# Optimization experiments

Measured on AMD Instinct MI355X. Metric: run time of the kernel, lower is better.

Reference implementation:

```python
import jax, jax.numpy as jnp
import numpy as np

COMMITMENT = 1.0


def setup_inputs() -> dict:
    key = jax.random.key(0)
    k1, k2 = jax.random.split(key)
    input = jax.random.normal(k1, (8, 64, 64, 256), dtype=jnp.float32)
    embed = jax.random.normal(k2, (256, 8192), dtype=jnp.float32)  # [dim, n_embed]
    return {"input": input, "embed": embed}


def reference(input, embed):
    dim = embed.shape[0]
    flatten = input.reshape(-1, dim)  # [N, dim]
    dist = (
        jnp.sum(flatten * flatten, axis=1, keepdims=True)
        - 2.0 * (flatten @ embed)
        + jnp.sum(embed * embed, axis=0, keepdims=True)
    )
    embed_ind = jnp.argmin(dist, axis=1)  # == (-dist).max(1) indices
    embed_ind = embed_ind.reshape(input.shape[:-1])  # [B, H, W]
    quantize = jnp.take(embed.T, embed_ind, axis=0)  # codebook lookup [B,H,W,dim]
    loss = jnp.mean((jax.lax.stop_gradient(quantize) - input) ** 2) * COMMITMENT
    quantize = input + jax.lax.stop_gradient(quantize - input)  # straight-through
    return quantize, embed_ind, loss
```

## Files before the change

kernel.cpp:

```cpp
#include <hip/hip_runtime.h>
#include <hip/hip_fp16.h>

#define NROW 32768
#define DIM  256
#define NC   8192
#define CAP  16384
#define MARGINF 0.25f
#define BIAS 512.0f
#define AST 576
#define BST 576
#define LOSS_SCALE (1.0f / 8388608.0f)

typedef __attribute__((ext_vector_type(8))) _Float16 half8;
typedef __attribute__((ext_vector_type(4))) _Float16 half4;
typedef __attribute__((ext_vector_type(4))) float   floatx4;
typedef const __attribute__((address_space(1))) void* gas_p;
typedef __attribute__((address_space(3))) void*       las_p;

static __device__ __forceinline__ unsigned short f2hb(float f) {
    _Float16 h = (_Float16)f;
    unsigned short u;
    __builtin_memcpy(&u, &h, 2);
    return u;
}
static __device__ __forceinline__ unsigned umin_(unsigned a, unsigned b) { return a < b ? a : b; }
static __device__ __forceinline__ unsigned umax_(unsigned a, unsigned b) { return a > b ? a : b; }


__global__ void prep_a_k(const float* __restrict__ x, unsigned short* __restrict__ Ah,
                         float* __restrict__ norms) {
    int row  = blockIdx.x * 4 + (threadIdx.x >> 6);
    int lane = threadIdx.x & 63;
    const float4 v = ((const float4*)(x + (size_t)row * DIM))[lane];
    float s = v.x * v.x + v.y * v.y + v.z * v.z + v.w * v.w;
#pragma unroll
    for (int off = 32; off; off >>= 1) s += __shfl_down(s, off, 64);
    if (lane == 0) norms[row] = s;
    ushort4 hi4 = make_ushort4(f2hb(v.x), f2hb(v.y), f2hb(v.z), f2hb(v.w));
    ushort4 lo4 = make_ushort4(f2hb(v.x - (float)(_Float16)v.x),
                               f2hb(v.y - (float)(_Float16)v.y),
                               f2hb(v.z - (float)(_Float16)v.z),
                               f2hb(v.w - (float)(_Float16)v.w));
    unsigned short* rp = Ah + (size_t)row * AST;
    *(ushort4*)(rp + lane * 4)       = hi4;
    *(ushort4*)(rp + 288 + lane * 4) = lo4;
    if (lane < 8) {
        ushort4 ob = make_ushort4(0, 0, 0, 0);
        if (lane == 0) { ob.x = 0x3C00; ob.y = 0x3C00; }
        *(ushort4*)(rp + 256 + lane * 4) = ob;
    }
}

__global__ void code_norms_k(const float* __restrict__ e, unsigned short* __restrict__ Bh,
                             float* __restrict__ cHalf) {
    int j = blockIdx.x * 256 + threadIdx.x;
    float s = 0.f;
    for (int d = 0; d < DIM; ++d) { float v = e[(size_t)d * NC + j]; s += v * v; }
    cHalf[j] = 0.5f * s;
    float t = -0.5f * s - BIAS;
    unsigned short hi = f2hb(t);
    _Float16 hf; __builtin_memcpy(&hf, &hi, 2);
    unsigned short lo = f2hb(t - (float)hf);
    unsigned short* p = Bh + (size_t)j * BST + 256;
    p[0] = hi; p[1] = lo;
    for (int k2 = 2; k2 < 32; ++k2) p[k2] = 0;
}

__global__ void prep_b_k(const float* __restrict__ e, unsigned short* __restrict__ Bh) {
    __shared__ float t[32][33];
    int jb = blockIdx.x * 32, db = blockIdx.y * 32;
#pragma unroll
    for (int i = 0; i < 4; ++i)
        t[threadIdx.y + i * 8][threadIdx.x] =
            e[(size_t)(db + threadIdx.y + i * 8) * NC + jb + threadIdx.x];
    __syncthreads();
#pragma unroll
    for (int i = 0; i < 4; ++i) {
        int j = jb + threadIdx.y + i * 8;
        int d = db + threadIdx.x;
        float val = t[threadIdx.x][threadIdx.y + i * 8];
        Bh[(size_t)j * BST + d]       = f2hb(val);
        Bh[(size_t)j * BST + 288 + d] = f2hb(val - (float)(_Float16)val);
    }
}


#define WAITBAR asm volatile("s_waitcnt vmcnt(2) lgkmcnt(4)\n\ts_barrier" ::: "memory")

__global__ __launch_bounds__(512, 2) void vq_cheap_k(
    const unsigned short* __restrict__ Ah, const unsigned short* __restrict__ Bh,
    const float* __restrict__ cHalf,
    float* __restrict__ pv, int* __restrict__ pj, float* __restrict__ psv)
{
    __shared__ __align__(16) _Float16 Asl[8][4096];
    __shared__ __align__(16) _Float16 Bsl[4][8192];
    __shared__ float chl[2048];

    const int tid  = threadIdx.x;
    const int js   = blockIdx.x & 3;
    const int rb   = blockIdx.x >> 2;
    const int row0 = rb * 128, col0 = js * 2048;
    const int lane = tid & 63, l15 = lane & 15, lq = lane >> 4;
    const int wave = tid >> 6;
    const int wr = (wave >> 2) * 64;
    const int wc = (wave & 3) * 64;
    const int sr = tid >> 2;
    const int ks = (((tid & 3) ^ (sr & 3) ^ ((sr >> 2) & 3))) * 8;

    {
        float4 a = ((const float4*)(cHalf + col0))[tid];
        a.x += BIAS; a.y += BIAS; a.z += BIAS; a.w += BIAS;
        ((float4*)chl)[tid] = a;
    }

    const unsigned short* Abase = Ah + (size_t)(row0 + sr) * AST + ks;
#pragma unroll
    for (int c = 0; c < 8; ++c)
        __builtin_amdgcn_global_load_lds((gas_p)(Abase + c * 32), (las_p)&Asl[c][tid * 8], 16, 0, 0);

#define LOADB(JT_, C_, BUF_)                                                                  \
    do {                                                                                      \
        const unsigned short* bb_ = Bh + (size_t)(col0 + (JT_) * 256 + sr) * BST + (C_) * 32 + ks; \
        _Float16* lb_ = &Bsl[(BUF_)][tid * 8];                                                \
        __builtin_amdgcn_global_load_lds((gas_p)bb_,               (las_p)lb_,          16, 0, 0); \
        __builtin_amdgcn_global_load_lds((gas_p)(bb_ + 128 * BST), (las_p)(lb_ + 4096), 16, 0, 0); \
    } while (0)

    LOADB(0, 0, 0);
    LOADB(0, 1, 1);
    LOADB(0, 2, 2);

    unsigned k1[16], k2[16];
#pragma unroll
    for (int s = 0; s < 16; ++s) { k1[s] = 0xFFFFFFFFu; k2[s] = 0xFFFFFFFFu; }

    const floatx4 fzero = {0.0f, 0.0f, 0.0f, 0.0f};
    floatx4 acc[4][4];
#pragma unroll
    for (int rf = 0; rf < 4; ++rf)
#pragma unroll
        for (int cf = 0; cf < 4; ++cf) acc[rf][cf] = fzero;

    WAITBAR;

    half8 ar[4][4];
#pragma unroll
    for (int c = 0; c < 4; ++c)
#pragma unroll
        for (int rf = 0; rf < 4; ++rf) {
            const int m = wr + rf * 16 + l15;
            const int g = lq ^ (m & 3) ^ ((m >> 2) & 3);
            ar[c][rf] = *(const half8*)&Asl[c][m * 32 + g * 8];
        }

    half8 af[4], bf[4];
#pragma unroll
    for (int cf = 0; cf < 4; ++cf) {
        const int n = wc + cf * 16 + l15;
        const int g = lq ^ (n & 3) ^ ((n >> 2) & 3);
        bf[cf] = *(const half8*)&Bsl[0][n * 32 + g * 8];
    }

    for (int jt = 0; jt < 8; ++jt) {
#pragma unroll
        for (int c = 0; c < 8; ++c) {
            if (c <= 4) LOADB(jt, c + 3, (c + 3) & 3);
            else        LOADB((jt + 1) & 7, c - 5, (c + 3) & 3);

            __builtin_amdgcn_s_setprio(1);
            if (c < 4) {
#pragma unroll
                for (int rf = 0; rf < 4; ++rf)
#pragma unroll
                    for (int cf = 0; cf < 4; ++cf)
                        acc[rf][cf] = __builtin_amdgcn_mfma_f32_16x16x32_f16(
                            ar[c][rf], bf[cf], acc[rf][cf], 0, 0, 0);
            } else {
#pragma unroll
                for (int rf = 0; rf < 4; ++rf)
#pragma unroll
                    for (int cf = 0; cf < 4; ++cf)
                        acc[rf][cf] = __builtin_amdgcn_mfma_f32_16x16x32_f16(
                            af[rf], bf[cf], acc[rf][cf], 0, 0, 0);
            }
            __builtin_amdgcn_s_setprio(0);
            __builtin_amdgcn_sched_barrier(0);

            if (c == 7) {
#pragma unroll
                for (int cf = 0; cf < 4; ++cf) {
                    const unsigned colb = (unsigned)(jt * 256 + wc + cf * 16 + l15);
                    const float ch = chl[colb];
#pragma unroll
                    for (int rf = 0; rf < 4; ++rf)
#pragma unroll
                        for (int r = 0; r < 4; ++r) {
                            float s = acc[rf][cf][r] - ch;
                            unsigned key = (__float_as_uint(s) & 0xFFFFF800u) | colb;
                            int slot = rf * 4 + r;
                            unsigned t = umax_(key, k1[slot]);
                            k1[slot] = umin_(k1[slot], key);
                            k2[slot] = umin_(k2[slot], t);
                        }
                }
#pragma unroll
                for (int rf = 0; rf < 4; ++rf)
#pragma unroll
                    for (int cf = 0; cf < 4; ++cf) acc[rf][cf] = fzero;
            }

            if (((c + 1) & 7) >= 4) {
#pragma unroll
                for (int rf = 0; rf < 4; ++rf) {
                    const int m = wr + rf * 16 + l15;
                    const int g = lq ^ (m & 3) ^ ((m >> 2) & 3);
                    af[rf] = *(const half8*)&Asl[(c + 1) & 7][m * 32 + g * 8];
                }
            }
#pragma unroll
            for (int cf = 0; cf < 4; ++cf) {
                const int n = wc + cf * 16 + l15;
                const int g = lq ^ (n & 3) ^ ((n >> 2) & 3);
                bf[cf] = *(const half8*)&Bsl[(c + 1) & 3][n * 32 + g * 8];
            }

            WAITBAR;
        }
    }
#undef LOADB

#pragma unroll
    for (int st = 1; st < 16; st <<= 1) {
#pragma unroll
        for (int s = 0; s < 16; ++s) {
            unsigned o1 = (unsigned)__shfl_xor((int)k1[s], st, 64);
            unsigned o2 = (unsigned)__shfl_xor((int)k2[s], st, 64);
            unsigned t = umax_(k1[s], o1);
            k1[s] = umin_(k1[s], o1);
            k2[s] = umin_(umin_(k2[s], o2), t);
        }
    }

    __syncthreads();
    unsigned* mk1 = (unsigned*)&Asl[0][0];
    unsigned* mk2 = (unsigned*)&Asl[1][0];
    if (l15 == 0) {
#pragma unroll
        for (int rf = 0; rf < 4; ++rf)
#pragma unroll
            for (int r = 0; r < 4; ++r) {
                int rloc = wr + rf * 16 + lq * 4 + r;
                int slot = rf * 4 + r;
                mk1[rloc * 4 + (wave & 3)] = k1[slot];
                mk2[rloc * 4 + (wave & 3)] = k2[slot];
            }
    }
    __syncthreads();
    if (tid < 128) {
        unsigned a0 = mk1[tid * 4], a1 = mk1[tid * 4 + 1], a2 = mk1[tid * 4 + 2], a3 = mk1[tid * 4 + 3];
        unsigned x = umin_(a0, a1), y = umax_(a0, a1);
        unsigned z = umin_(a2, a3), w = umax_(a2, a3);
        unsigned m1  = umin_(x, z);
        unsigned sm1 = umin_(umax_(x, z), umin_(y, w));
        unsigned s0 = mk2[tid * 4], s1 = mk2[tid * 4 + 1], s2 = mk2[tid * 4 + 2], s3 = mk2[tid * 4 + 3];
        unsigned m2 = umin_(umin_(umin_(s0, s1), umin_(s2, s3)), sm1);
        pv[(size_t)js * NROW + row0 + tid]  = __uint_as_float(m1 & 0xFFFFF800u);
        pj[(size_t)js * NROW + row0 + tid]  = (int)(m1 & 2047u) + js * 2048;
        psv[(size_t)js * NROW + row0 + tid] = __uint_as_float(m2 & 0xFFFFF800u);
    }
}

#undef WAITBAR


template<bool RESCUE>
static __device__ __forceinline__ void chunk_off(int c, int& ac, int& bc) {
    if constexpr (RESCUE) {
        if (c < 8)       { ac = c * 32;              bc = c * 32; }
        else if (c < 16) { ac = (c - 8) * 32;        bc = 288 + (c - 8) * 32; }
        else             { ac = 288 + (c - 16) * 32; bc = (c - 16) * 32; }
    } else {
        ac = c * 32; bc = c * 32;
    }
}

template<int CHUNKS, int JT, int JSB, bool RESCUE>
__global__ __launch_bounds__(256, 2) void vq_gemm_k(
    const unsigned short* __restrict__ Ah, const unsigned short* __restrict__ Bh,
    const float* __restrict__ cHalf,
    float* __restrict__ pv, int* __restrict__ pj, float* __restrict__ psv,
    const int* __restrict__ list, const int* __restrict__ cnt)
{
    __shared__ __align__(16) _Float16 As[2][4096];
    __shared__ __align__(16) _Float16 Bs[2][4096];

    const int tid  = threadIdx.x;
    const int js   = blockIdx.x & ((1 << JSB) - 1);
    const int rb   = blockIdx.x >> JSB;
    const int row0 = rb * 128, col0 = js * (JT * 128);
    const int lane = tid & 63, l15 = lane & 15, lq = lane >> 4;
    const int wave = tid >> 6;
    const int wrow = (wave >> 1) * 64, wcol = (wave & 1) * 64;
    const int sr = tid >> 2, sp = (tid & 3) * 8;

    int nact = 0;
    if constexpr (RESCUE) {
        nact = *cnt;
        if (row0 >= nact) return;
    }

    const unsigned short *Abase0, *Abase1;
    if constexpr (RESCUE) {
        int i0 = row0 + sr, i1 = i0 + 64;
        int r0 = (i0 < nact) ? list[i0] : 0;
        int r1 = (i1 < nact) ? list[i1] : 0;
        Abase0 = Ah + (size_t)r0 * AST + sp;
        Abase1 = Ah + (size_t)r1 * AST + sp;
    } else {
        Abase0 = Ah + (size_t)(row0 + sr) * AST + sp;
        Abase1 = Abase0 + 64 * AST;
    }

    unsigned k1[16], k2[16];
    float bvf[16]; int bjf[16];
#pragma unroll
    for (int s = 0; s < 16; ++s) {
        k1[s] = 0xFFFFFFFFu; k2[s] = 0xFFFFFFFFu;
        bvf[s] = -3.4e38f; bjf[s] = 0;
    }

    const floatx4 fzero = {0.0f, 0.0f, 0.0f, 0.0f};
    floatx4 acc[4][4];
#pragma unroll
    for (int rf = 0; rf < 4; ++rf)
#pragma unroll
        for (int cf = 0; cf < 4; ++cf) acc[rf][cf] = fzero;

    const unsigned short* Bb = Bh + (size_t)(col0 + sr) * BST + sp;

#define LOAD4(AC, BC, BUF, BBASE)                                                            \
    do {                                                                                     \
        _Float16* la_ = &As[(BUF)][tid * 8];                                                 \
        _Float16* lb_ = &Bs[(BUF)][tid * 8];                                                 \
        __builtin_amdgcn_global_load_lds((gas_p)(Abase0 + (AC)),            (las_p)la_,          16, 0, 0); \
        __builtin_amdgcn_global_load_lds((gas_p)(Abase1 + (AC)),            (las_p)(la_ + 2048), 16, 0, 0); \
        __builtin_amdgcn_global_load_lds((gas_p)((BBASE) + (BC)),           (las_p)lb_,          16, 0, 0); \
        __builtin_amdgcn_global_load_lds((gas_p)((BBASE) + 64 * BST + (BC)),(las_p)(lb_ + 2048), 16, 0, 0); \
    } while (0)

    LOAD4(0, 0, 0, Bb);

    for (int jt = 0; jt < JT; ++jt) {
        const int p = (CHUNKS & 1) ? (jt & 1) : 0;
#pragma unroll
        for (int c = 0; c < CHUNKS; ++c) {
            const int buf = (c & 1) ^ p;
            __syncthreads();
            if (c + 1 < CHUNKS) {
                int an, bn;
                chunk_off<RESCUE>(c + 1, an, bn);
                LOAD4(an, bn, buf ^ 1, Bb);
            } else if (jt + 1 < JT) {
                LOAD4(0, 0, buf ^ 1, Bb + 128 * BST);
            }

            half8 af[4], bf[4];
#pragma unroll
            for (int rf = 0; rf < 4; ++rf)
                af[rf] = *(const half8*)&As[buf][(wrow + rf * 16 + l15) * 32 + lq * 8];
#pragma unroll
            for (int cf = 0; cf < 4; ++cf)
                bf[cf] = *(const half8*)&Bs[buf][(wcol + cf * 16 + l15) * 32 + lq * 8];
#pragma unroll
            for (int rf = 0; rf < 4; ++rf)
#pragma unroll
                for (int cf = 0; cf < 4; ++cf)
                    acc[rf][cf] = __builtin_amdgcn_mfma_f32_16x16x32_f16(
                        af[rf], bf[cf], acc[rf][cf], 0, 0, 0);

            if (c == CHUNKS - 1) {
                if constexpr (RESCUE) {
                    const int colbase = col0 + jt * 128 + wcol;
#pragma unroll
                    for (int cf = 0; cf < 4; ++cf) {
                        const int col = colbase + cf * 16 + l15;
                        const float ch = cHalf[col];
#pragma unroll
                        for (int rf = 0; rf < 4; ++rf)
#pragma unroll
                            for (int r = 0; r < 4; ++r) {
                                float s = acc[rf][cf][r] - ch;
                                int slot = rf * 4 + r;
                                if (s > bvf[slot]) { bvf[slot] = s; bjf[slot] = col; }
                            }
                    }
                } else {
                    const unsigned colloc = (unsigned)(jt * 128 + wcol);
#pragma unroll
                    for (int cf = 0; cf < 4; ++cf) {
                        const unsigned colb = colloc + cf * 16 + l15;
#pragma unroll
                        for (int rf = 0; rf < 4; ++rf)
#pragma unroll
                            for (int r = 0; r < 4; ++r) {
                                unsigned key = (__float_as_uint(acc[rf][cf][r]) & 0xFFFFF800u) | colb;
                                int slot = rf * 4 + r;
                                unsigned t = umax_(key, k1[slot]);
                                k1[slot] = umin_(k1[slot], key);
                                k2[slot] = umin_(k2[slot], t);
                            }
                    }
                }
#pragma unroll
                for (int rf = 0; rf < 4; ++rf)
#pragma unroll
                    for (int cf = 0; cf < 4; ++cf) acc[rf][cf] = fzero;
            }
        }
        Bb += 128 * BST;
    }
#undef LOAD4

#pragma unroll
    for (int st = 1; st < 16; st <<= 1) {
#pragma unroll
        for (int s = 0; s < 16; ++s) {
            if constexpr (RESCUE) {
                float v2 = __shfl_xor(bvf[s], st, 64);
                int   j2 = __shfl_xor(bjf[s], st, 64);
                if (v2 > bvf[s] || (v2 == bvf[s] && j2 < bjf[s])) { bvf[s] = v2; bjf[s] = j2; }
            } else {
                unsigned o1 = (unsigned)__shfl_xor((int)k1[s], st, 64);
                unsigned o2 = (unsigned)__shfl_xor((int)k2[s], st, 64);
                unsigned t = umax_(k1[s], o1);
                k1[s] = umin_(k1[s], o1);
                k2[s] = umin_(umin_(k2[s], o2), t);
            }
        }
    }

    __syncthreads();
    if constexpr (RESCUE) {
        float* mv = (float*)&As[0][0];
        int*   mj = (int*)&Bs[0][0];
        if (l15 == 0) {
#pragma unroll
            for (int rf = 0; rf < 4; ++rf)
#pragma unroll
                for (int r = 0; r < 4; ++r) {
                    int rloc = wrow + rf * 16 + lq * 4 + r;
                    int slot = rf * 4 + r;
                    mv[rloc * 2 + (wave & 1)] = bvf[slot];
                    mj[rloc * 2 + (wave & 1)] = bjf[slot];
                }
        }
        __syncthreads();
        if (tid < 128) {
            float v0 = mv[tid * 2], v1 = mv[tid * 2 + 1];
            int   j0 = mj[tid * 2], j1 = mj[tid * 2 + 1];
            bool take1 = (v1 > v0) || (v1 == v0 && j1 < j0);
            pv[(size_t)js * CAP + row0 + tid] = take1 ? v1 : v0;
            pj[(size_t)js * CAP + row0 + tid] = take1 ? j1 : j0;
        }
    } else {
        unsigned* mk1 = (unsigned*)&As[0][0];
        unsigned* mk2 = (unsigned*)&Bs[0][0];
        if (l15 == 0) {
#pragma unroll
            for (int rf = 0; rf < 4; ++rf)
#pragma unroll
                for (int r = 0; r < 4; ++r) {
                    int rloc = wrow + rf * 16 + lq * 4 + r;
                    int slot = rf * 4 + r;
                    mk1[rloc * 2 + (wave & 1)] = k1[slot];
                    mk2[rloc * 2 + (wave & 1)] = k2[slot];
                }
        }
        __syncthreads();
        if (tid < 128) {
            unsigned a1 = mk1[tid * 2], b1 = mk1[tid * 2 + 1];
            unsigned a2 = mk2[tid * 2], b2 = mk2[tid * 2 + 1];
            unsigned m1 = umin_(a1, b1);
            unsigned m2 = umin_(umin_(a2, b2), umax_(a1, b1));
            pv[(size_t)js * NROW + row0 + tid] = __uint_as_float(m1 & 0xFFFFF800u);
            pj[(size_t)js * NROW + row0 + tid] = (int)(m1 & 2047u) + js * (JT * 128);
            psv[(size_t)js * NROW + row0 + tid] = __uint_as_float(m2 & 0xFFFFF800u);
        }
    }
}


__global__ void vq_reduce_k(const float* __restrict__ pv, const int* __restrict__ pj,
                            const float* __restrict__ psv,
                            const float* __restrict__ norms, const unsigned short* __restrict__ Bh,
                            float* __restrict__ qout, float* __restrict__ iout,
                            float* __restrict__ lout, int* __restrict__ list,
                            int* __restrict__ cnt)
{
    __shared__ int jbuf[64];
    const int row0 = blockIdx.x * 64;
    const int tid = threadIdx.x;
    if (tid < 64) {
        int row = row0 + tid;
        float bv = pv[row]; int bj = pj[row]; float sv = psv[row];
#pragma unroll
        for (int s = 1; s < 4; ++s) {
            float v = pv[(size_t)s * NROW + row];
            int   j = pj[(size_t)s * NROW + row];
            float s2 = psv[(size_t)s * NROW + row];
            bool better = (v > bv) || (v == bv && j < bj);
            float loseBest = better ? bv : v;
            sv = fmaxf(fmaxf(sv, s2), loseBest);
            if (better) { bv = v; bj = j; }
        }
        bool flagged = (bv - sv) < MARGINF;
        if (flagged) {
            int idx = atomicAdd(cnt, 1);
            if (idx < CAP) {
                list[idx] = row;
                jbuf[tid] = -1;
            } else {
                flagged = false;
            }
        }
        float rl = 0.f;
        if (!flagged) {
            iout[row] = (float)bj;
            jbuf[tid] = bj;
            rl = norms[row] - 2.0f * (bv + BIAS - 0.0625f);
        }
#pragma unroll
        for (int off = 32; off; off >>= 1) rl += __shfl_down(rl, off, 64);
        if (tid == 0) atomicAdd(lout, rl * LOSS_SCALE);
    }
    __syncthreads();
    const int lane = tid & 63;
    for (int r = tid >> 6; r < 64; r += 4) {
        int j = jbuf[r];
        if (j >= 0) {
            const _Float16* bp = (const _Float16*)Bh + (size_t)j * BST + lane * 4;
            half4 h = *(const half4*)bp;
            half4 l = *(const half4*)(bp + 288);
            float4 v;
            v.x = (float)h[0] + (float)l[0];
            v.y = (float)h[1] + (float)l[1];
            v.z = (float)h[2] + (float)l[2];
            v.w = (float)h[3] + (float)l[3];
            *(float4*)&qout[(size_t)(row0 + r) * DIM + lane * 4] = v;
        }
    }
}


__global__ void vq_reduce2_k(const float* __restrict__ pv2, const int* __restrict__ pj2,
                             const int* __restrict__ list, const int* __restrict__ cnt,
                             const float* __restrict__ norms, const unsigned short* __restrict__ Bh,
                             float* __restrict__ qout, float* __restrict__ iout,
                             float* __restrict__ lout)
{
    __shared__ int rbuf[64], jb2[64];
    const int n = *cnt < CAP ? *cnt : CAP;
    const int i0 = blockIdx.x * 64;
    if (i0 >= n) return;
    const int tid = threadIdx.x;
    if (tid < 64) {
        int i = i0 + tid;
        float rl = 0.f;
        if (i < n) {
            float bv = pv2[i]; int bj = pj2[i];
#pragma unroll 4
            for (int s = 1; s < 32; ++s) {
                float v = pv2[(size_t)s * CAP + i];
                int   j = pj2[(size_t)s * CAP + i];
                if (v > bv || (v == bv && j < bj)) { bv = v; bj = j; }
            }
            int row = list[i];
            iout[row] = (float)bj;
            rbuf[tid] = row;
            jb2[tid]  = bj;
            rl = norms[row] - 2.0f * bv;
        } else {
            rbuf[tid] = -1;
        }
#pragma unroll
        for (int off = 32; off; off >>= 1) rl += __shfl_down(rl, off, 64);
        if (tid == 0) atomicAdd(lout, rl * LOSS_SCALE);
    }
    __syncthreads();
    const int lane = tid & 63;
    for (int r = tid >> 6; r < 64; r += 4) {
        int row = rbuf[r];
        if (row >= 0) {
            const _Float16* bp = (const _Float16*)Bh + (size_t)jb2[r] * BST + lane * 4;
            half4 h = *(const half4*)bp;
            half4 l = *(const half4*)(bp + 288);
            float4 v;
            v.x = (float)h[0] + (float)l[0];
            v.y = (float)h[1] + (float)l[1];
            v.z = (float)h[2] + (float)l[2];
            v.w = (float)h[3] + (float)l[3];
            *(float4*)&qout[(size_t)row * DIM + lane * 4] = v;
        }
    }
}


__global__ void transpose_k(const float* __restrict__ e, float* __restrict__ eT) {
    __shared__ float t[32][33];
    int jb = blockIdx.x * 32, db = blockIdx.y * 32;
#pragma unroll
    for (int i = 0; i < 4; ++i)
        t[threadIdx.y + i * 8][threadIdx.x] =
            e[(size_t)(db + threadIdx.y + i * 8) * NC + jb + threadIdx.x];
    __syncthreads();
#pragma unroll
    for (int i = 0; i < 4; ++i)
        eT[(size_t)(jb + threadIdx.y + i * 8) * DIM + db + threadIdx.x] =
            t[threadIdx.x][threadIdx.y + i * 8];
}

__global__ void row_norms_k(const float* __restrict__ x, float* __restrict__ norms) {
    int row  = blockIdx.x * 4 + (threadIdx.x >> 6);
    int lane = threadIdx.x & 63;
    const float4 v = ((const float4*)(x + (size_t)row * DIM))[lane];
    float s = v.x * v.x + v.y * v.y + v.z * v.z + v.w * v.w;
#pragma unroll
    for (int off = 32; off; off >>= 1) s += __shfl_down(s, off, 64);
    if (lane == 0) norms[row] = s;
}

__global__ void code_norms_fb_k(const float* __restrict__ e, float* __restrict__ cHalf) {
    int j = blockIdx.x * 256 + threadIdx.x;
    float s = 0.f;
    for (int d = 0; d < DIM; ++d) { float v = e[(size_t)d * NC + j]; s += v * v; }
    cHalf[j] = 0.5f * s;
}

__global__ __launch_bounds__(256, 4) void vq_main_k(
    const float* __restrict__ x, const float* __restrict__ e,
    const float* __restrict__ eT, const float* __restrict__ norms,
    const float* __restrict__ cHalf, float* __restrict__ qout,
    float* __restrict__ iout, float* __restrict__ lout, int useT)
{
    __shared__ float  As[2][32 * 68];
    __shared__ float4 Bs[2][512];
    const int tid  = threadIdx.x;
    const int row0 = blockIdx.x * 64;
    const int ty = tid >> 4, tx = tid & 15;
    const int ar = tid >> 2, ak = (tid & 3) * 4;
    const int bk = tid >> 4, bj = tid & 15;
    float bestv[4]; int bestj[4];
#pragma unroll
    for (int i = 0; i < 4; ++i) { bestv[i] = -3.4e38f; bestj[i] = 0; }
    float acc[4][4];
    float4 pa0, pa1, pb0, pb1;
    {
        const float* xp = x + (size_t)(row0 + ar) * DIM + ak;
        pa0 = *(const float4*)xp;
        pa1 = *(const float4*)(xp + 16);
        const float* ep = e + (size_t)bk * NC + bj * 4;
        pb0 = *(const float4*)ep;
        pb1 = *(const float4*)(ep + 16 * NC);
    }
    int buf = 0;
    for (int c = 0; c < 1024; ++c) {
        const int kc = c & 7;
#pragma unroll
        for (int q = 0; q < 4; ++q) As[buf][(ak + q) * 68 + ar]      = ((const float*)&pa0)[q];
#pragma unroll
        for (int q = 0; q < 4; ++q) As[buf][(16 + ak + q) * 68 + ar] = ((const float*)&pa1)[q];
        Bs[buf][bk * 16 + bj]        = pb0;
        Bs[buf][(bk + 16) * 16 + bj] = pb1;
        __syncthreads();
        if (c + 1 < 1024) {
            int j0n  = ((c + 1) >> 3) * 64;
            int kk0n = ((c + 1) & 7) * 32;
            const float* xp = x + (size_t)(row0 + ar) * DIM + kk0n + ak;
            pa0 = *(const float4*)xp;
            pa1 = *(const float4*)(xp + 16);
            const float* ep = e + (size_t)(kk0n + bk) * NC + j0n + bj * 4;
            pb0 = *(const float4*)ep;
            pb1 = *(const float4*)(ep + 16 * NC);
        }
        if (kc == 0) {
#pragma unroll
            for (int i = 0; i < 4; ++i)
#pragma unroll
                for (int j = 0; j < 4; ++j) acc[i][j] = 0.f;
        }
#pragma unroll
        for (int k = 0; k < 32; ++k) {
            float4 a = *(const float4*)&As[buf][k * 68 + ty * 4];
            float4 b = *(const float4*)&Bs[buf][k * 16 + tx];
            acc[0][0] += a.x * b.x; acc[0][1] += a.x * b.y; acc[0][2] += a.x * b.z; acc[0][3] += a.x * b.w;
            acc[1][0] += a.y * b.x; acc[1][1] += a.y * b.y; acc[1][2] += a.y * b.z; acc[1][3] += a.y * b.w;
            acc[2][0] += a.z * b.x; acc[2][1] += a.z * b.y; acc[2][2] += a.z * b.z; acc[2][3] += a.z * b.w;
            acc[3][0] += a.w * b.x; acc[3][1] += a.w * b.y; acc[3][2] += a.w * b.z; acc[3][3] += a.w * b.w;
        }
        if (kc == 7) {
            int j0 = (c >> 3) * 64;
            float4 ch = *(const float4*)&cHalf[j0 + tx * 4];
            int jb0 = j0 + tx * 4;
#pragma unroll
            for (int i = 0; i < 4; ++i)
#pragma unroll
                for (int j = 0; j < 4; ++j) {
                    float s = acc[i][j] - ((const float*)&ch)[j];
                    if (s > bestv[i]) { bestv[i] = s; bestj[i] = jb0 + j; }
                }
        }
        buf ^= 1;
    }
    __syncthreads();
    float* redv   = &As[0][0];
    int*   redj   = (int*)&As[0][1024];
    int*   idxbuf = (int*)&As[1][0];
#pragma unroll
    for (int i = 0; i < 4; ++i) {
        int r = ty * 4 + i;
        redv[r * 16 + tx] = bestv[i];
        redj[r * 16 + tx] = bestj[i];
    }
    __syncthreads();
    if (tid < 64) {
        float bvv = redv[tid * 16];
        int   bj2 = redj[tid * 16];
#pragma unroll
        for (int t = 1; t < 16; ++t) {
            float v = redv[tid * 16 + t];
            int   j = redj[tid * 16 + t];
            if (v > bvv || (v == bvv && j < bj2)) { bvv = v; bj2 = j; }
        }
        iout[row0 + tid] = (float)bj2;
        idxbuf[tid] = bj2;
        float rl = norms[row0 + tid] - 2.0f * bvv;
#pragma unroll
        for (int off = 32; off; off >>= 1) rl += __shfl_down(rl, off, 64);
        if (tid == 0) atomicAdd(lout, rl * LOSS_SCALE);
    }
    __syncthreads();
    {
        const int rr = tid >> 6, lane = tid & 63;
        for (int r = rr; r < 64; r += 4) {
            int j = idxbuf[r];
            float4 v;
            if (useT) {
                v = *(const float4*)&eT[(size_t)j * DIM + lane * 4];
            } else {
                int d = lane * 4;
                v.x = e[(size_t)d * NC + j];
                v.y = e[(size_t)(d + 1) * NC + j];
                v.z = e[(size_t)(d + 2) * NC + j];
                v.w = e[(size_t)(d + 3) * NC + j];
            }
            *(float4*)&qout[(size_t)(row0 + r) * DIM + lane * 4] = v;
        }
    }
}


extern "C" void kernel_launch(void* const* d_in, const int* in_sizes, int n_in,
                              void* d_out, int out_size, void* d_ws, size_t ws_size,
                              hipStream_t stream) {
    const float* x = (const float*)d_in[0];
    const float* e = (const float*)d_in[1];

    float* qout = (float*)d_out;
    float* iout = qout + (size_t)NROW * DIM;
    float* lout = iout + NROW;

    char* ws = (char*)d_ws;
    const size_t offAh    = 0;
    const size_t offBh    = offAh + 37748736;
    const size_t offNorms = offBh + 9437184;
    const size_t offCH    = offNorms + 131072;
    const size_t offPV    = offCH + 32768;
    const size_t offPJ    = offPV + 524288;
    const size_t offPSV   = offPJ + 524288;
    const size_t offPV2   = offPSV + 524288;
    const size_t offPJ2   = offPV2 + 2097152;
    const size_t offList  = offPJ2 + 2097152;
    const size_t offCnt   = offList + 65536;
    const size_t needFast = offCnt + 256;

    hipMemsetAsync(lout, 0, sizeof(float), stream);

    if (ws_size >= needFast) {
        unsigned short* Ah = (unsigned short*)(ws + offAh);
        unsigned short* Bh = (unsigned short*)(ws + offBh);
        float* norms = (float*)(ws + offNorms);
        float* cHalf = (float*)(ws + offCH);
        float* pv    = (float*)(ws + offPV);
        int*   pj    = (int*)(ws + offPJ);
        float* psv   = (float*)(ws + offPSV);
        float* pv2   = (float*)(ws + offPV2);
        int*   pj2   = (int*)(ws + offPJ2);
        int*   list  = (int*)(ws + offList);
        int*   cnt   = (int*)(ws + offCnt);

        hipMemsetAsync(cnt, 0, sizeof(int), stream);
        prep_a_k<<<NROW / 4, 256, 0, stream>>>(x, Ah, norms);
        code_norms_k<<<NC / 256, 256, 0, stream>>>(e, Bh, cHalf);
        prep_b_k<<<dim3(NC / 32, DIM / 32), dim3(32, 8), 0, stream>>>(e, Bh);
        vq_cheap_k<<<1024, 512, 0, stream>>>(Ah, Bh, cHalf, pv, pj, psv);
        vq_reduce_k<<<NROW / 64, 256, 0, stream>>>(
            pv, pj, psv, norms, Bh, qout, iout, lout, list, cnt);
        vq_gemm_k<24, 2, 5, true><<<(CAP / 128) * 32, 256, 0, stream>>>(
            Ah, Bh, cHalf, pv2, pj2, nullptr, list, cnt);
        vq_reduce2_k<<<CAP / 64, 256, 0, stream>>>(
            pv2, pj2, list, cnt, norms, Bh, qout, iout, lout);
    } else {
        float* fws   = (float*)d_ws;
        float* norms = fws;
        float* cHalf = fws + NROW;
        float* eT    = fws + NROW + NC;
        size_t need_T = (size_t)(NROW + NC) * sizeof(float) + (size_t)NC * DIM * sizeof(float);
        int useT = (ws_size >= need_T) ? 1 : 0;
        row_norms_k<<<NROW / 4, 256, 0, stream>>>(x, norms);
        code_norms_fb_k<<<NC / 256, 256, 0, stream>>>(e, cHalf);
        if (useT)
            transpose_k<<<dim3(NC / 32, DIM / 32), dim3(32, 8), 0, stream>>>(e, eT);
        vq_main_k<<<NROW / 64, 256, 0, stream>>>(x, e, eT, norms, cHalf, qout, iout, lout, useT);
    }
}
```

Before: 344.8 us.

## Give each wave private B staging buffers and drop per-chunk block barriers

The cheap-pass GEMM kernel now has each wave stage its own 64-column slice of the codebook into a private triple-buffered LDS region. This removes the workgroup-wide s_barrier after every K chunk, so waves only wait on their own vmcnt and lgkmcnt. The first four A chunks are loaded into a scratch area that is later reused for B and held in registers, which lets the A LDS buffer shrink. In exchange, B tiles that were shared across waves are loaded redundantly by each wave sharing the same column slice, which raises global and L2 traffic. Waves may also drift apart from each other.

```diff
diff --git a/kernel.cpp b/kernel.cpp
--- a/kernel.cpp
+++ b/kernel.cpp
@@ -85,15 +85,13 @@
 }
 
 
-#define WAITBAR asm volatile("s_waitcnt vmcnt(2) lgkmcnt(4)\n\ts_barrier" ::: "memory")
-
 __global__ __launch_bounds__(512, 2) void vq_cheap_k(
     const unsigned short* __restrict__ Ah, const unsigned short* __restrict__ Bh,
     const float* __restrict__ cHalf,
     float* __restrict__ pv, int* __restrict__ pj, float* __restrict__ psv)
 {
-    __shared__ __align__(16) _Float16 Asl[8][4096];
-    __shared__ __align__(16) _Float16 Bsl[4][8192];
+    __shared__ __align__(16) _Float16 Asl[4][4096];
+    __shared__ __align__(16) _Float16 Bw[8][3][2048];
     __shared__ float chl[2048];
 
     const int tid  = threadIdx.x;
@@ -107,6 +105,13 @@
     const int sr = tid >> 2;
     const int ks = (((tid & 3) ^ (sr & 3) ^ ((sr >> 2) & 3))) * 8;
 
+    const int colq = lane >> 2;
+    const int pq   = lane & 3;
+    const int sgS  = (colq & 3) ^ ((colq >> 2) & 3);
+    const int gS   = (pq ^ sgS) * 8;
+    const int sR   = (l15 & 3) ^ ((l15 >> 2) & 3);
+    const int roB  = l15 * 32 + ((lq ^ sR) * 8);
+
     {
         float4 a = ((const float4*)(cHalf + col0))[tid];
         a.x += BIAS; a.y += BIAS; a.z += BIAS; a.w += BIAS;
@@ -114,34 +119,16 @@
     }
 
     const unsigned short* Abase = Ah + (size_t)(row0 + sr) * AST + ks;
-#pragma unroll
-    for (int c = 0; c < 8; ++c)
-        __builtin_amdgcn_global_load_lds((gas_p)(Abase + c * 32), (las_p)&Asl[c][tid * 8], 16, 0, 0);
-
-#define LOADB(JT_, C_, BUF_)                                                                  \
-    do {                                                                                      \
-        const unsigned short* bb_ = Bh + (size_t)(col0 + (JT_) * 256 + sr) * BST + (C_) * 32 + ks; \
-        _Float16* lb_ = &Bsl[(BUF_)][tid * 8];                                                \
-        __builtin_amdgcn_global_load_lds((gas_p)bb_,               (las_p)lb_,          16, 0, 0); \
-        __builtin_amdgcn_global_load_lds((gas_p)(bb_ + 128 * BST), (las_p)(lb_ + 4096), 16, 0, 0); \
-    } while (0)
-
-    LOADB(0, 0, 0);
-    LOADB(0, 1, 1);
-    LOADB(0, 2, 2);
-
-    unsigned k1[16], k2[16];
-#pragma unroll
-    for (int s = 0; s < 16; ++s) { k1[s] = 0xFFFFFFFFu; k2[s] = 0xFFFFFFFFu; }
-
-    const floatx4 fzero = {0.0f, 0.0f, 0.0f, 0.0f};
-    floatx4 acc[4][4];
-#pragma unroll
-    for (int rf = 0; rf < 4; ++rf)
-#pragma unroll
-        for (int cf = 0; cf < 4; ++cf) acc[rf][cf] = fzero;
-
-    WAITBAR;
+    _Float16* Ascr = &Bw[0][0][0];
+#pragma unroll
+    for (int c = 0; c < 4; ++c)
+        __builtin_amdgcn_global_load_lds((gas_p)(Abase + (c + 4) * 32), (las_p)&Asl[c][tid * 8], 16, 0, 0);
+#pragma unroll
+    for (int c = 0; c < 4; ++c)
+        __builtin_amdgcn_global_load_lds((gas_p)(Abase + c * 32), (las_p)&Ascr[c * 4096 + tid * 8], 16, 0, 0);
+
+    asm volatile("s_waitcnt vmcnt(0) lgkmcnt(0)" ::: "memory");
+    __builtin_amdgcn_s_barrier();
 
     half8 ar[4][4];
 #pragma unroll
@@ -150,22 +137,65 @@
         for (int rf = 0; rf < 4; ++rf) {
             const int m = wr + rf * 16 + l15;
             const int g = lq ^ (m & 3) ^ ((m >> 2) & 3);
-            ar[c][rf] = *(const half8*)&Asl[c][m * 32 + g * 8];
-        }
+            ar[c][rf] = *(const half8*)&Ascr[c * 4096 + m * 32 + g * 8];
+        }
+    asm volatile("s_waitcnt lgkmcnt(0)" ::: "memory");
+    __builtin_amdgcn_s_barrier();
+
+    const unsigned short* Bbase = Bh + (size_t)(col0 + wc + colq) * BST + gS;
+#define STAGEB(JT_, C_, SLOT_)                                                                \
+    do {                                                                                      \
+        const unsigned short* b0_ = Bbase + (size_t)(JT_) * (256 * BST) + (C_) * 32;          \
+        _Float16* d0_ = &Bw[wave][(SLOT_)][lane * 8];                                         \
+        __builtin_amdgcn_global_load_lds((gas_p)(b0_),                (las_p)(d0_),          16, 0, 0); \
+        __builtin_amdgcn_global_load_lds((gas_p)(b0_ + 16 * BST),     (las_p)(d0_ + 512),    16, 0, 0); \
+        __builtin_amdgcn_global_load_lds((gas_p)(b0_ + 32 * BST),     (las_p)(d0_ + 1024),   16, 0, 0); \
+        __builtin_amdgcn_global_load_lds((gas_p)(b0_ + 48 * BST),     (las_p)(d0_ + 1536),   16, 0, 0); \
+    } while (0)
+
+    STAGEB(0, 0, 0);
+    STAGEB(0, 1, 1);
+    STAGEB(0, 2, 2);
+
+    unsigned k1[16], k2[16];
+#pragma unroll
+    for (int s = 0; s < 16; ++s) { k1[s] = 0xFFFFFFFFu; k2[s] = 0xFFFFFFFFu; }
+
+    const floatx4 fzero = {0.0f, 0.0f, 0.0f, 0.0f};
+    floatx4 acc[4][4];
+#pragma unroll
+    for (int rf = 0; rf < 4; ++rf)
+#pragma unroll
+        for (int cf = 0; cf < 4; ++cf) acc[rf][cf] = fzero;
 
     half8 af[4], bf[4];
-#pragma unroll
-    for (int cf = 0; cf < 4; ++cf) {
-        const int n = wc + cf * 16 + l15;
-        const int g = lq ^ (n & 3) ^ ((n >> 2) & 3);
-        bf[cf] = *(const half8*)&Bsl[0][n * 32 + g * 8];
-    }
+    int slot = 0;
 
     for (int jt = 0; jt < 8; ++jt) {
 #pragma unroll
         for (int c = 0; c < 8; ++c) {
-            if (c <= 4) LOADB(jt, c + 3, (c + 3) & 3);
-            else        LOADB((jt + 1) & 7, c - 5, (c + 3) & 3);
+            asm volatile("s_waitcnt vmcnt(8)" ::: "memory");
+
+            if (c >= 4) {
+#pragma unroll
+                for (int rf = 0; rf < 4; ++rf) {
+                    const int m = wr + rf * 16 + l15;
+                    const int g = lq ^ (m & 3) ^ ((m >> 2) & 3);
+                    af[rf] = *(const half8*)&Asl[c - 4][m * 32 + g * 8];
+                }
+            }
+#pragma unroll
+            for (int cf = 0; cf < 4; ++cf)
+                bf[cf] = *(const half8*)&Bw[wave][slot][cf * 512 + roB];
+
+            asm volatile("s_waitcnt lgkmcnt(0)" ::: "memory");
+            __builtin_amdgcn_sched_barrier(0);
+            {
+                const int T   = jt * 8 + c + 3;
+                const int jtn = (T >> 3) & 7;
+                const int cn  = T & 7;
+                STAGEB(jtn, cn, slot);
+            }
 
             __builtin_amdgcn_s_setprio(1);
             if (c < 4) {
@@ -184,7 +214,6 @@
                             af[rf], bf[cf], acc[rf][cf], 0, 0, 0);
             }
             __builtin_amdgcn_s_setprio(0);
-            __builtin_amdgcn_sched_barrier(0);
 
             if (c == 7) {
 #pragma unroll
@@ -197,10 +226,10 @@
                         for (int r = 0; r < 4; ++r) {
                             float s = acc[rf][cf][r] - ch;
                             unsigned key = (__float_as_uint(s) & 0xFFFFF800u) | colb;
-                            int slot = rf * 4 + r;
-                            unsigned t = umax_(key, k1[slot]);
-                            k1[slot] = umin_(k1[slot], key);
-                            k2[slot] = umin_(k2[slot], t);
+                            int slot2 = rf * 4 + r;
+                            unsigned t = umax_(key, k1[slot2]);
+                            k1[slot2] = umin_(k1[slot2], key);
+                            k2[slot2] = umin_(k2[slot2], t);
                         }
                 }
 #pragma unroll
@@ -209,25 +238,10 @@
                     for (int cf = 0; cf < 4; ++cf) acc[rf][cf] = fzero;
             }
 
-            if (((c + 1) & 7) >= 4) {
-#pragma unroll
-                for (int rf = 0; rf < 4; ++rf) {
-                    const int m = wr + rf * 16 + l15;
-                    const int g = lq ^ (m & 3) ^ ((m >> 2) & 3);
-                    af[rf] = *(const half8*)&Asl[(c + 1) & 7][m * 32 + g * 8];
-                }
-            }
-#pragma unroll
-            for (int cf = 0; cf < 4; ++cf) {
-                const int n = wc + cf * 16 + l15;
-                const int g = lq ^ (n & 3) ^ ((n >> 2) & 3);
-                bf[cf] = *(const half8*)&Bsl[(c + 1) & 3][n * 32 + g * 8];
-            }
-
-            WAITBAR;
-        }
-    }
-#undef LOADB
+            slot = (slot == 2) ? 0 : slot + 1;
+        }
+    }
+#undef STAGEB
 
 #pragma unroll
     for (int st = 1; st < 16; st <<= 1) {
@@ -250,9 +264,9 @@
 #pragma unroll
             for (int r = 0; r < 4; ++r) {
                 int rloc = wr + rf * 16 + lq * 4 + r;
-                int slot = rf * 4 + r;
-                mk1[rloc * 4 + (wave & 3)] = k1[slot];
-                mk2[rloc * 4 + (wave & 3)] = k2[slot];
+                int s2 = rf * 4 + r;
+                mk1[rloc * 4 + (wave & 3)] = k1[s2];
+                mk2[rloc * 4 + (wave & 3)] = k2[s2];
             }
     }
     __syncthreads();
@@ -269,8 +283,6 @@
         psv[(size_t)js * NROW + row0 + tid] = __uint_as_float(m2 & 0xFFFFF800u);
     }
 }
-
-#undef WAITBAR
 
 
 template<bool RESCUE>
```

Measured after the change: 373.2 us. 1.08x slower.
